# Kernel tuning notes

Measured on AMD Instinct MI355X. Metric: run time of the kernel, lower is better.

## Reference

```python
import jax, jax.numpy as jnp
import numpy as np

PAD_MAG = 1e12
EPS = 1e-7  # matches prev_step.add_(1e-07) in the torch code


def setup_inputs() -> dict:
    key = jax.random.key(0)
    k1, k2, k3, k4 = jax.random.split(key, 4)
    B, txt_T, mel_T, n_mel = 16, 320, 2000, 80
    mu_logvar = jax.random.normal(k1, (B, txt_T, 2 * n_mel), dtype=jnp.float32)
    melspec = jax.random.normal(k2, (B, n_mel, mel_T), dtype=jnp.float32)
    text_lengths = jax.random.randint(k3, (B,), txt_T // 2, txt_T + 1).astype(jnp.int32)
    mel_lengths = jax.random.randint(k4, (B,), mel_T // 2, mel_T + 1).astype(jnp.int32)
    return {"mu_logvar": mu_logvar, "melspec": melspec,
            "text_lengths": text_lengths, "mel_lengths": mel_lengths}


def _log_prob_matrix(mu_logvar, melspec):
    # exponential[b,j,t] = -0.5 * mean_c( (x[b,t,c]-mu[b,j,c])^2 / exp(logvar) + logvar )
    # avoiding the [B,txt_T,mel_T,n_mel] broadcast the torch code materializes.
    n_mel = melspec.shape[1]
    mu = mu_logvar[:, :, :n_mel]          # [B, txt_T, n_mel]
    logvar = mu_logvar[:, :, n_mel:]      # [B, txt_T, n_mel]
    x = jnp.swapaxes(melspec, 1, 2)       # [B, mel_T, n_mel]
    inv_var = jnp.exp(-logvar)
    xx = jnp.einsum('btc,bjc->bjt', x * x, inv_var)
    xm = jnp.einsum('btc,bjc->bjt', x, mu * inv_var)
    mm = jnp.sum(mu * mu * inv_var + logvar, axis=2)  # [B, txt_T]
    return (-0.5 / n_mel) * (xx - 2.0 * xm + mm[:, :, None])  # [B, txt_T, mel_T]


def _forward_dp(log_prob, text_lengths, mel_lengths):
    # monotonic alignment forward algorithm (logsumexp DP over mel frames)
    B, txt_T, mel_T = log_prob.shape
    # carry = log_alpha column of size txt_T+1 (row 0 is the -inf pad row)
    init = jnp.full((B, txt_T + 1), -PAD_MAG, log_prob.dtype)
    init = init.at[:, 1].set(log_prob[:, 0, 0])

    def step(a, lp):  # a: [B, txt_T+1], lp: [B, txt_T]
        prev = jnp.stack([a[:, 1:], a[:, :-1]], axis=-1) + EPS
        tail = jax.nn.logsumexp(prev, axis=-1) + lp      # [B, txt_T]
        a_new = jnp.concatenate(
            [jnp.full((B, 1), -PAD_MAG, a.dtype), tail], axis=1)
        return a_new, tail

    lps = jnp.moveaxis(log_prob[:, :, 1:], 2, 0)         # [mel_T-1, B, txt_T]
    _, tails = jax.lax.scan(step, init, lps)             # [mel_T-1, B, txt_T]
    log_alpha = jnp.concatenate([init[None, :, 1:], tails], axis=0)  # [mel_T, B, txt_T]
    log_alpha = jnp.moveaxis(log_alpha, 0, 2)            # [B, txt_T, mel_T]

    bidx = jnp.arange(B)
    alpha_last = log_alpha[bidx, text_lengths - 1, mel_lengths - 1]
    alpha_last = alpha_last / mel_lengths.astype(log_alpha.dtype)
    return -jnp.mean(alpha_last)


def reference(mu_logvar, melspec, text_lengths, mel_lengths):
    log_prob = _log_prob_matrix(mu_logvar, melspec)
    mdn_loss = _forward_dp(log_prob, text_lengths, mel_lengths)
    return (mdn_loss, log_prob)
```

## Files before the change

### kernel.cpp

```cpp
#include <hip/hip_runtime.h>

#define BATCH 16
#define TXT   320
#define NMELC 80
#define MELT  2000
#define PADM  1.0e12f
#define EPSC  1e-7f
#define L2E   1.4426950408889634f
#define LN2   0.6931471805599453f
#define EPSL2 1.4426950e-7f

__global__ __launch_bounds__(256) void lp_kernel(
    const float* __restrict__ mlv,
    const float* __restrict__ ms,
    float* __restrict__ out_lp)
{
    __shared__ float Gt[16][64];
    __shared__ float Ft[16][256];
    __shared__ float bias_s[64];
    __shared__ float bias_p[256];

    const int b   = blockIdx.z;
    const int j0  = blockIdx.y * 64;
    const int t0  = blockIdx.x * 256;
    const int tid = threadIdx.x;
    const float s = -0.00625f;

    const float* mlv_b = mlv + (size_t)b * TXT * 160;
    const float* ms_b  = ms  + (size_t)b * NMELC * MELT;

    {
        const int jj = tid >> 2;
        const int q  = tid & 3;
        const float* p = mlv_b + (size_t)(j0 + jj) * 160 + q * 20;
        float part = 0.f;
        #pragma unroll
        for (int c = 0; c < 20; ++c) {
            float mu = p[c];
            float lv = p[c + 80];
            float iv = __expf(-lv);
            part += mu * mu * iv + lv;
        }
        bias_p[tid] = part;
    }
    __syncthreads();
    if (tid < 64) {
        float v = bias_p[tid * 4] + bias_p[tid * 4 + 1] +
                  bias_p[tid * 4 + 2] + bias_p[tid * 4 + 3];
        bias_s[tid] = s * v;
    }

    float acc[8][8];
    #pragma unroll
    for (int i = 0; i < 8; ++i)
        #pragma unroll
        for (int k = 0; k < 8; ++k) acc[i][k] = 0.f;

    const int jg = tid >> 5;
    const int tg = tid & 31;

    for (int kc = 0; kc < 10; ++kc) {
        const int c0 = kc * 8;
        __syncthreads();
        #pragma unroll
        for (int i = 0; i < 2; ++i) {
            int f   = tid + i * 256;
            int cr  = f >> 6;
            int col = f & 63;
            float mu = mlv_b[(size_t)(j0 + col) * 160 + (c0 + cr)];
            float lv = mlv_b[(size_t)(j0 + col) * 160 + (80 + c0 + cr)];
            float iv = __expf(-lv);
            Gt[cr][col]     = s * iv;
            Gt[cr + 8][col] = -2.f * s * mu * iv;
        }
        #pragma unroll
        for (int i = 0; i < 2; ++i) {
            int f   = tid + i * 256;
            int row = f >> 6;
            int c4  = f & 63;
            int t   = t0 + c4 * 4;
            float4 v = (t + 3 < MELT)
                ? *(const float4*)&ms_b[(size_t)(c0 + row) * MELT + t]
                : make_float4(0.f, 0.f, 0.f, 0.f);
            *(float4*)&Ft[row][c4 * 4] =
                make_float4(v.x * v.x, v.y * v.y, v.z * v.z, v.w * v.w);
            *(float4*)&Ft[row + 8][c4 * 4] = v;
        }
        __syncthreads();
        #pragma unroll
        for (int k = 0; k < 16; ++k) {
            float4 g0 = *(const float4*)&Gt[k][jg * 8];
            float4 g1 = *(const float4*)&Gt[k][jg * 8 + 4];
            float4 f0 = *(const float4*)&Ft[k][tg * 8];
            float4 f1 = *(const float4*)&Ft[k][tg * 8 + 4];
            float ga[8] = {g0.x, g0.y, g0.z, g0.w, g1.x, g1.y, g1.z, g1.w};
            float fa[8] = {f0.x, f0.y, f0.z, f0.w, f1.x, f1.y, f1.z, f1.w};
            #pragma unroll
            for (int ji = 0; ji < 8; ++ji)
                #pragma unroll
                for (int ti = 0; ti < 8; ++ti)
                    acc[ji][ti] = fmaf(ga[ji], fa[ti], acc[ji][ti]);
        }
    }

    #pragma unroll
    for (int ji = 0; ji < 8; ++ji) {
        int j = j0 + jg * 8 + ji;
        float bs = bias_s[jg * 8 + ji];
        float* orow = out_lp + (size_t)(b * TXT + j) * MELT;
        #pragma unroll
        for (int ti = 0; ti < 8; ++ti) {
            int t = t0 + tg * 8 + ti;
            if (t < MELT) orow[t] = acc[ji][ti] + bs;
        }
    }
}

__device__ __forceinline__ float dpp_shr1(float x) {
    return __int_as_float(__builtin_amdgcn_update_dpp(
        0, __float_as_int(x), 0x138 , 0xF, 0xF, false));
}

__global__ __launch_bounds__(192, 1) void dp_kernel(
    const float* __restrict__ lp,
    const int* __restrict__ tlen,
    const int* __restrict__ mlen,
    float* __restrict__ res,
    float* __restrict__ out0)
{
    __shared__ float bnd[2][2056];
    __shared__ int   prog[2];

    const int b    = blockIdx.x;
    const int tid  = threadIdx.x;
    const int w    = tid >> 6;
    const int l    = tid & 63;
    const int tend = mlen[b] - 1;
    const int tl   = tlen[b];

    if (tid < 2) prog[tid] = 0;

    int j0c = 2 * tid; if (j0c > 318) j0c = 318;
    const float* r0 = lp + (size_t)(b * TXT + j0c) * MELT;
    const float* r1 = r0 + MELT;

    float A1 = (tid == 0) ? lp[(size_t)b * TXT * MELT] * L2E : -PADM;
    float A2 = -PADM;
    float A1F = A1, A2F = A2;

    if (l == 63 && w < 2) bnd[w][0] = -PADM;
    __syncthreads();

    if (w == 2 && tl < 257) return;

    float ptA2 = -PADM, ptB2 = -PADM;
    const bool is0     = (l == 0);
    const bool isPub   = (l == 63) && (w < 2);
    const bool hasRing = (w > 0);
    int seen = 0;

    const int imax = tend + 63;

    float PA[16], PB[16], PC[16];
    #pragma unroll
    for (int q = 0; q < 8; ++q) { PA[2*q] = r0[1 + q - l]; PA[2*q+1] = r1[1 + q - l]; }
    #pragma unroll
    for (int q = 0; q < 8; ++q) { PB[2*q] = r0[9 + q - l]; PB[2*q+1] = r1[9 + q - l]; }
    #pragma unroll
    for (int q = 0; q < 16; ++q) PA[q] = fmaf(PA[q], L2E, EPSL2);

    const float* p0 = r0 + 17 - l;
    const float* p1 = r1 + 17 - l;

#define RING_RD(BQ_, T0_)                                                    \
    {                                                                        \
        float4 r0_ = *(const float4*)&bnd[w - 1][T0_];                       \
        float4 r1_ = *(const float4*)&bnd[w - 1][(T0_) + 4];                 \
        BQ_[0]=r0_.x; BQ_[1]=r0_.y; BQ_[2]=r0_.z; BQ_[3]=r0_.w;              \
        BQ_[4]=r1_.x; BQ_[5]=r1_.y; BQ_[6]=r1_.z; BQ_[7]=r1_.w;              \
    }
#define RING_POLL(NEED_)                                                     \
    if (seen < (NEED_)) {                                                    \
        int tgt_ = (NEED_) + 32;                                             \
        if (tgt_ > tend - 1) tgt_ = tend - 1;                                \
        if (tgt_ < (NEED_)) tgt_ = (NEED_);                                  \
        volatile int* pv_ = &prog[w - 1];                                    \
        int v_ = *pv_;                                                       \
        while (v_ < tgt_) { __builtin_amdgcn_s_sleep(1); v_ = *pv_; }        \
        seen = v_;                                                           \
        __asm__ volatile("" ::: "memory");                                   \
    }

    float bqC[8];
    if (hasRing) {
        RING_POLL(7)
        RING_RD(bqC, 0)
    } else {
        #pragma unroll
        for (int q = 0; q < 8; ++q) bqC[q] = -PADM;
    }

#define STEP2(Pc_, q_, AQ_)                                                  \
    {                                                                        \
        float pt_ = is0 ? bqC[q_] : ptA2;                                    \
        float m1_ = fmaxf(A1, pt_);                                          \
        float d1_ = A1 - pt_;                                                \
        float e1_ = __builtin_amdgcn_exp2f(-fabsf(d1_));                     \
        float g1_ = __builtin_amdgcn_logf(1.0f + e1_);                       \
        float n1_ = m1_ + g1_ + Pc_[2 * q_];                                 \
        float m2_ = fmaxf(A2, A1);                                           \
        float d2_ = A2 - A1;                                                 \
        float e2_ = __builtin_amdgcn_exp2f(-fabsf(d2_));                     \
        float g2_ = __builtin_amdgcn_logf(1.0f + e2_);                       \
        float n2_ = m2_ + g2_ + Pc_[2 * q_ + 1];                             \
        float ns_ = dpp_shr1(n2_);                                           \
        ptA2 = ptB2; ptB2 = ns_;                                             \
        A1 = n1_; A2 = n2_; AQ_ = n2_;                                       \
    }

#define GROUP2_S(Pc_, Pm_, Pl_, I0_)                                         \
{                                                                            \
    float bqN[8];                                                            \
    if (hasRing) {                                                           \
        const int nt0_ = (I0_) + 7;                                          \
        RING_POLL(nt0_ + 7)                                                  \
        RING_RD(bqN, nt0_)                                                   \
    } else {                                                                 \
        _Pragma("unroll") for (int q_=0;q_<8;++q_) bqN[q_] = -PADM;          \
    }                                                                        \
    _Pragma("unroll") for (int q_=0;q_<8;++q_) {                             \
        Pl_[2*q_] = p0[q_]; Pl_[2*q_+1] = p1[q_];                            \
    }                                                                        \
    float aq2[8];                                                            \
    _Pragma("unroll")                                                        \
    for (int q_=0;q_<8;++q_) STEP2(Pc_, q_, aq2[q_])                         \
    if (isPub) {                                                             \
        const int t63_ = (I0_) - 63;                                         \
        if (t63_ >= 1) {                                                     \
            _Pragma("unroll") for (int q_=0;q_<8;++q_)                       \
                bnd[w][t63_ + q_] = aq2[q_];                                 \
        } else {                                                             \
            _Pragma("unroll") for (int q_=0;q_<8;++q_)                       \
                if (t63_ + q_ >= 1) bnd[w][t63_ + q_] = aq2[q_];             \
        }                                                                    \
        __asm__ volatile("" ::: "memory");          \
        int pgv_ = t63_ + 7;                                                 \
        if (pgv_ >= 1) prog[w] = pgv_;                                       \
    }                                                                        \
    p0 += 8; p1 += 8;                                                        \
    _Pragma("unroll") for (int q_=0;q_<16;++q_)                              \
        Pm_[q_] = fmaf(Pm_[q_], L2E, EPSL2);                                 \
    _Pragma("unroll") for (int q_=0;q_<8;++q_) bqC[q_] = bqN[q_];            \
}

#define GROUP2_T(Pc_, Pm_, Pl_, I0_)                                         \
{                                                                            \
    float bqN[8];                                                            \
    if (hasRing) {                                                           \
        const int nt0_ = (I0_) + 7;                                          \
        int need_ = nt0_ + 7; if (need_ > tend - 1) need_ = tend - 1;        \
        RING_POLL(need_)                                                     \
        const int rb_ = nt0_ > 2048 ? 2048 : nt0_;                           \
        RING_RD(bqN, rb_)                                                    \
    } else {                                                                 \
        _Pragma("unroll") for (int q_=0;q_<8;++q_) bqN[q_] = -PADM;          \
    }                                                                        \
    _Pragma("unroll") for (int q_=0;q_<8;++q_) {                             \
        int t_ = (I0_) + 16 + q_ - l;                                        \
        t_ = t_ < 0 ? 0 : (t_ > tend ? tend : t_);                           \
        Pl_[2*q_] = r0[t_]; Pl_[2*q_+1] = r1[t_];                            \
    }                                                                        \
    float aq2[8];                                                            \
    const int vt_ = (I0_) - l;                                               \
    _Pragma("unroll")                                                        \
    for (int q_=0;q_<8;++q_) {                                               \
        STEP2(Pc_, q_, aq2[q_])                                              \
        bool c_ = (vt_ + q_ == tend);                                        \
        A1F = c_ ? A1 : A1F;                                                 \
        A2F = c_ ? A2 : A2F;                                                 \
    }                                                                        \
    if (isPub) {                                                             \
        const int t63_ = (I0_) - 63;                                         \
        _Pragma("unroll") for (int q_=0;q_<8;++q_) {                         \
            int tq_ = t63_ + q_;                                             \
            if (tq_ >= 1 && tq_ <= tend) bnd[w][tq_] = aq2[q_];              \
        }                                                                    \
        __asm__ volatile("" ::: "memory");                                   \
        int pgv_ = t63_ + 7; if (pgv_ > tend) pgv_ = tend;                   \
        if (pgv_ >= 1) prog[w] = pgv_;                                       \
    }                                                                        \
    _Pragma("unroll") for (int q_=0;q_<16;++q_)                              \
        Pm_[q_] = fmaf(Pm_[q_], L2E, EPSL2);                                 \
    _Pragma("unroll") for (int q_=0;q_<8;++q_) bqC[q_] = bqN[q_];            \
}

    int i0 = 1;
    const int sEnd = tend - 23;
    int ph = 0;
    while (i0 <= sEnd) {
        GROUP2_S(PA, PB, PC, i0); i0 += 8;
        if (i0 > sEnd) { ph = 1; break; }
        GROUP2_S(PB, PC, PA, i0); i0 += 8;
        if (i0 > sEnd) { ph = 2; break; }
        GROUP2_S(PC, PA, PB, i0); i0 += 8;
    }
    if (ph == 1) {
        #pragma unroll
        for (int q = 0; q < 16; ++q) {
            float tmp = PA[q]; PA[q] = PB[q]; PB[q] = PC[q]; PC[q] = tmp;
        }
    } else if (ph == 2) {
        #pragma unroll
        for (int q = 0; q < 16; ++q) {
            float tmp = PA[q]; PA[q] = PC[q]; PC[q] = PB[q]; PB[q] = tmp;
        }
    }
    while (i0 <= imax) {
        GROUP2_T(PA, PB, PC, i0); i0 += 8;
        if (i0 > imax) break;
        GROUP2_T(PB, PC, PA, i0); i0 += 8;
        if (i0 > imax) break;
        GROUP2_T(PC, PA, PB, i0); i0 += 8;
    }

#undef GROUP2_S
#undef GROUP2_T
#undef STEP2
#undef RING_RD
#undef RING_POLL

    if (tid == ((tl - 1) >> 1)) {
        float Af = ((tl - 1) & 1) ? A2F : A1F;
        float v = Af * LN2 / (float)(tend + 1);
        if (res) res[b] = v;
        else     atomicAdd(out0, -v / (float)BATCH);
    }
}

__global__ void zero1_kernel(float* out0) { out0[0] = 0.f; }

__global__ void fin_kernel(const float* __restrict__ res, float* __restrict__ out0)
{
    int l = threadIdx.x;
    float v = (l < BATCH) ? res[l] : 0.f;
    #pragma unroll
    for (int off = 32; off; off >>= 1) v += __shfl_down(v, off);
    if (l == 0) out0[0] = -(v / (float)BATCH);
}

extern "C" void kernel_launch(void* const* d_in, const int* in_sizes, int n_in,
                              void* d_out, int out_size, void* d_ws, size_t ws_size,
                              hipStream_t stream)
{
    const float* mlv = (const float*)d_in[0];
    const float* ms  = (const float*)d_in[1];
    const int*   tl  = (const int*)d_in[2];
    const int*   ml  = (const int*)d_in[3];
    float* out    = (float*)d_out;
    float* out_lp = out + 1;

    bool res_ok = ws_size >= 64;
    float* res = res_ok ? (float*)d_ws : nullptr;

    dim3 gA(8, 5, 16);
    lp_kernel<<<gA, 256, 0, stream>>>(mlv, ms, out_lp);

    if (!res_ok) zero1_kernel<<<1, 1, 0, stream>>>(out);
    dp_kernel<<<BATCH, 192, 0, stream>>>(out_lp, tl, ml, res, out);
    if (res_ok) fin_kernel<<<1, 64, 0, stream>>>(res, out);
}
```

Measured before the change: 244.7 us.

## Split DP into forward and backward half passes meeting in the middle

Replaces the single sequential forward DP per batch with two concurrent passes: a forward pass over the first half of mel frames and a backward pass from the end over the second half. A small kernel then combines the two half-results with a logsumexp over text positions. This roughly halves the serial chain length of the latency-bound DP and doubles the blocks from 16 to 32. The cost is extra workspace, two extra small kernels, and added numerical/indexing risk in the reverse-pass initialization and the boundary subtraction.

```diff
diff --git a/kernel.cpp b/kernel.cpp
--- a/kernel.cpp
+++ b/kernel.cpp
@@ -5,7 +5,6 @@
 #define NMELC 80
 #define MELT  2000
 #define PADM  1.0e12f
-#define EPSC  1e-7f
 #define L2E   1.4426950408889634f
 #define LN2   0.6931471805599453f
 #define EPSL2 1.4426950e-7f
@@ -121,68 +120,81 @@
         0, __float_as_int(x), 0x138 , 0xF, 0xF, false));
 }
 
-__global__ __launch_bounds__(192, 1) void dp_kernel(
-    const float* __restrict__ lp,
-    const int* __restrict__ tlen,
-    const int* __restrict__ mlen,
-    float* __restrict__ res,
-    float* __restrict__ out0)
-{
-    __shared__ float bnd[2][2056];
+__device__ __forceinline__ void dp_pass(
+    const float* __restrict__ lp, int b, int dir, int tend, int tl,
+    float* __restrict__ Fout, float* __restrict__ out0)
+{
+    __shared__ float bnd[2][2080];
     __shared__ int   prog[2];
 
-    const int b    = blockIdx.x;
-    const int tid  = threadIdx.x;
-    const int w    = tid >> 6;
-    const int l    = tid & 63;
-    const int tend = mlen[b] - 1;
-    const int tl   = tlen[b];
+    const int tid = threadIdx.x;
+    const int w   = tid >> 6;
+    const int l   = tid & 63;
+    const int tm    = tend >> 1;
+    const int steps = Fout ? (dir ? (tend - tm) : tm) : tend;
+    const int t0c   = dir ? tend : 0;
+    const int dsgn  = dir ? -1 : 1;
 
     if (tid < 2) prog[tid] = 0;
 
-    int j0c = 2 * tid; if (j0c > 318) j0c = 318;
-    const float* r0 = lp + (size_t)(b * TXT + j0c) * MELT;
-    const float* r1 = r0 + MELT;
-
-    float A1 = (tid == 0) ? lp[(size_t)b * TXT * MELT] * L2E : -PADM;
-    float A2 = -PADM;
+    const int tc = tid < 160 ? tid : 159;
+    const int R0 = dir ? (319 - 2 * tc) : (2 * tc);
+    const int R1 = dir ? (318 - 2 * tc) : (2 * tc + 1);
+    const float* r0 = lp + ((size_t)b * TXT + R0) * MELT;
+    const float* r1 = lp + ((size_t)b * TXT + R1) * MELT;
+
+    float A1 = -PADM, A2 = -PADM;
+    if (!dir) {
+        if (tid == 0) A1 = lp[(size_t)b * TXT * MELT] * L2E;
+    } else {
+        const int jin = 320 - tl;
+        const float vin =
+            fmaf(lp[((size_t)b * TXT + (tl - 1)) * MELT + tend], L2E, EPSL2);
+        if (tid == (jin >> 1)) { if (jin & 1) A2 = vin; else A1 = vin; }
+    }
     float A1F = A1, A2F = A2;
 
-    if (l == 63 && w < 2) bnd[w][0] = -PADM;
+    if (l == 63 && w < 2) bnd[w][0] = A2;
     __syncthreads();
-
-    if (w == 2 && tl < 257) return;
-
-    float ptA2 = -PADM, ptB2 = -PADM;
+    if (tid >= 192) return;
+
+    float ptA2 = -PADM;
+    float ptB2 = dpp_shr1(A2);
     const bool is0     = (l == 0);
     const bool isPub   = (l == 63) && (w < 2);
     const bool hasRing = (w > 0);
     int seen = 0;
-
-    const int imax = tend + 63;
+    const int imax = steps + 63;
 
     float PA[16], PB[16], PC[16];
     #pragma unroll
-    for (int q = 0; q < 8; ++q) { PA[2*q] = r0[1 + q - l]; PA[2*q+1] = r1[1 + q - l]; }
-    #pragma unroll
-    for (int q = 0; q < 8; ++q) { PB[2*q] = r0[9 + q - l]; PB[2*q+1] = r1[9 + q - l]; }
+    for (int q = 0; q < 8; ++q) {
+        int s_ = 1 + q - l;
+        int c_ = t0c + dsgn * s_;
+        c_ = c_ < 0 ? 0 : (c_ > MELT - 1 ? MELT - 1 : c_);
+        PA[2 * q] = r0[c_]; PA[2 * q + 1] = r1[c_];
+    }
+    #pragma unroll
+    for (int q = 0; q < 8; ++q) {
+        int s_ = 9 + q - l;
+        int c_ = t0c + dsgn * s_;
+        c_ = c_ < 0 ? 0 : (c_ > MELT - 1 ? MELT - 1 : c_);
+        PB[2 * q] = r0[c_]; PB[2 * q + 1] = r1[c_];
+    }
     #pragma unroll
     for (int q = 0; q < 16; ++q) PA[q] = fmaf(PA[q], L2E, EPSL2);
-
-    const float* p0 = r0 + 17 - l;
-    const float* p1 = r1 + 17 - l;
 
 #define RING_RD(BQ_, T0_)                                                    \
     {                                                                        \
-        float4 r0_ = *(const float4*)&bnd[w - 1][T0_];                       \
-        float4 r1_ = *(const float4*)&bnd[w - 1][(T0_) + 4];                 \
-        BQ_[0]=r0_.x; BQ_[1]=r0_.y; BQ_[2]=r0_.z; BQ_[3]=r0_.w;              \
-        BQ_[4]=r1_.x; BQ_[5]=r1_.y; BQ_[6]=r1_.z; BQ_[7]=r1_.w;              \
+        float4 q0_ = *(const float4*)&bnd[w - 1][T0_];                       \
+        float4 q1_ = *(const float4*)&bnd[w - 1][(T0_) + 4];                 \
+        BQ_[0]=q0_.x; BQ_[1]=q0_.y; BQ_[2]=q0_.z; BQ_[3]=q0_.w;              \
+        BQ_[4]=q1_.x; BQ_[5]=q1_.y; BQ_[6]=q1_.z; BQ_[7]=q1_.w;              \
     }
 #define RING_POLL(NEED_)                                                     \
     if (seen < (NEED_)) {                                                    \
         int tgt_ = (NEED_) + 32;                                             \
-        if (tgt_ > tend - 1) tgt_ = tend - 1;                                \
+        if (tgt_ > steps - 1) tgt_ = steps - 1;                              \
         if (tgt_ < (NEED_)) tgt_ = (NEED_);                                  \
         volatile int* pv_ = &prog[w - 1];                                    \
         int v_ = *pv_;                                                       \
@@ -193,100 +205,65 @@
 
     float bqC[8];
     if (hasRing) {
-        RING_POLL(7)
+        int need0 = 7; if (need0 > steps - 1) need0 = steps - 1;
+        RING_POLL(need0)
         RING_RD(bqC, 0)
     } else {
         #pragma unroll
         for (int q = 0; q < 8; ++q) bqC[q] = -PADM;
     }
 
-#define STEP2(Pc_, q_, AQ_)                                                  \
-    {                                                                        \
+#define GROUPX(Pc_, Pm_, Pl_, I0_)                                           \
+{                                                                            \
+    float bqN[8];                                                            \
+    if (hasRing) {                                                           \
+        int need_ = (I0_) + 14;                                              \
+        if (need_ > steps - 1) need_ = steps - 1;                            \
+        RING_POLL(need_)                                                     \
+        int rb_ = (I0_) + 7; if (rb_ > 2048) rb_ = 2048;                     \
+        RING_RD(bqN, rb_)                                                    \
+    } else {                                                                 \
+        _Pragma("unroll") for (int q_=0;q_<8;++q_) bqN[q_] = -PADM;          \
+    }                                                                        \
+    _Pragma("unroll") for (int q_=0;q_<8;++q_) {                             \
+        int s_ = (I0_) + 16 + q_ - l;                                        \
+        int c_ = t0c + dsgn * s_;                                            \
+        c_ = c_ < 0 ? 0 : (c_ > MELT - 1 ? MELT - 1 : c_);                   \
+        Pl_[2*q_] = r0[c_]; Pl_[2*q_+1] = r1[c_];                            \
+    }                                                                        \
+    float aq2[8];                                                            \
+    const int vt_ = (I0_) - l;                                               \
+    _Pragma("unroll") for (int q_=0;q_<8;++q_) {                             \
         float pt_ = is0 ? bqC[q_] : ptA2;                                    \
         float m1_ = fmaxf(A1, pt_);                                          \
         float d1_ = A1 - pt_;                                                \
         float e1_ = __builtin_amdgcn_exp2f(-fabsf(d1_));                     \
         float g1_ = __builtin_amdgcn_logf(1.0f + e1_);                       \
-        float n1_ = m1_ + g1_ + Pc_[2 * q_];                                 \
+        float n1_ = m1_ + g1_ + Pc_[2*q_];                                   \
         float m2_ = fmaxf(A2, A1);                                           \
         float d2_ = A2 - A1;                                                 \
         float e2_ = __builtin_amdgcn_exp2f(-fabsf(d2_));                     \
         float g2_ = __builtin_amdgcn_logf(1.0f + e2_);                       \
-        float n2_ = m2_ + g2_ + Pc_[2 * q_ + 1];                             \
-        float ns_ = dpp_shr1(n2_);                                           \
+        float n2_ = m2_ + g2_ + Pc_[2*q_+1];                                 \
+        bool go_ = (vt_ + q_ >= 1);                                          \
+        A1 = go_ ? n1_ : A1;                                                 \
+        A2 = go_ ? n2_ : A2;                                                 \
+        float ns_ = dpp_shr1(A2);                                            \
         ptA2 = ptB2; ptB2 = ns_;                                             \
-        A1 = n1_; A2 = n2_; AQ_ = n2_;                                       \
-    }
-
-#define GROUP2_S(Pc_, Pm_, Pl_, I0_)                                         \
-{                                                                            \
-    float bqN[8];                                                            \
-    if (hasRing) {                                                           \
-        const int nt0_ = (I0_) + 7;                                          \
-        RING_POLL(nt0_ + 7)                                                  \
-        RING_RD(bqN, nt0_)                                                   \
-    } else {                                                                 \
-        _Pragma("unroll") for (int q_=0;q_<8;++q_) bqN[q_] = -PADM;          \
-    }                                                                        \
-    _Pragma("unroll") for (int q_=0;q_<8;++q_) {                             \
-        Pl_[2*q_] = p0[q_]; Pl_[2*q_+1] = p1[q_];                            \
-    }                                                                        \
-    float aq2[8];                                                            \
-    _Pragma("unroll")                                                        \
-    for (int q_=0;q_<8;++q_) STEP2(Pc_, q_, aq2[q_])                         \
-    if (isPub) {                                                             \
-        const int t63_ = (I0_) - 63;                                         \
-        if (t63_ >= 1) {                                                     \
-            _Pragma("unroll") for (int q_=0;q_<8;++q_)                       \
-                bnd[w][t63_ + q_] = aq2[q_];                                 \
-        } else {                                                             \
-            _Pragma("unroll") for (int q_=0;q_<8;++q_)                       \
-                if (t63_ + q_ >= 1) bnd[w][t63_ + q_] = aq2[q_];             \
-        }                                                                    \
-        __asm__ volatile("" ::: "memory");          \
-        int pgv_ = t63_ + 7;                                                 \
-        if (pgv_ >= 1) prog[w] = pgv_;                                       \
-    }                                                                        \
-    p0 += 8; p1 += 8;                                                        \
-    _Pragma("unroll") for (int q_=0;q_<16;++q_)                              \
-        Pm_[q_] = fmaf(Pm_[q_], L2E, EPSL2);                                 \
-    _Pragma("unroll") for (int q_=0;q_<8;++q_) bqC[q_] = bqN[q_];            \
-}
-
-#define GROUP2_T(Pc_, Pm_, Pl_, I0_)                                         \
-{                                                                            \
-    float bqN[8];                                                            \
-    if (hasRing) {                                                           \
-        const int nt0_ = (I0_) + 7;                                          \
-        int need_ = nt0_ + 7; if (need_ > tend - 1) need_ = tend - 1;        \
-        RING_POLL(need_)                                                     \
-        const int rb_ = nt0_ > 2048 ? 2048 : nt0_;                           \
-        RING_RD(bqN, rb_)                                                    \
-    } else {                                                                 \
-        _Pragma("unroll") for (int q_=0;q_<8;++q_) bqN[q_] = -PADM;          \
-    }                                                                        \
-    _Pragma("unroll") for (int q_=0;q_<8;++q_) {                             \
-        int t_ = (I0_) + 16 + q_ - l;                                        \
-        t_ = t_ < 0 ? 0 : (t_ > tend ? tend : t_);                           \
-        Pl_[2*q_] = r0[t_]; Pl_[2*q_+1] = r1[t_];                            \
-    }                                                                        \
-    float aq2[8];                                                            \
-    const int vt_ = (I0_) - l;                                               \
-    _Pragma("unroll")                                                        \
-    for (int q_=0;q_<8;++q_) {                                               \
-        STEP2(Pc_, q_, aq2[q_])                                              \
-        bool c_ = (vt_ + q_ == tend);                                        \
-        A1F = c_ ? A1 : A1F;                                                 \
-        A2F = c_ ? A2 : A2F;                                                 \
+        aq2[q_] = A2;                                                        \
+        bool cF_ = (vt_ + q_ == steps);                                      \
+        A1F = cF_ ? A1 : A1F;                                                \
+        A2F = cF_ ? A2 : A2F;                                                \
     }                                                                        \
     if (isPub) {                                                             \
         const int t63_ = (I0_) - 63;                                         \
         _Pragma("unroll") for (int q_=0;q_<8;++q_) {                         \
             int tq_ = t63_ + q_;                                             \
-            if (tq_ >= 1 && tq_ <= tend) bnd[w][tq_] = aq2[q_];              \
+            if (tq_ >= 1 && tq_ <= 2056) bnd[w][tq_] = aq2[q_];              \
         }                                                                    \
         __asm__ volatile("" ::: "memory");                                   \
-        int pgv_ = t63_ + 7; if (pgv_ > tend) pgv_ = tend;                   \
+        int pgv_ = t63_ + 7;                                                 \
+        if (pgv_ > steps - 1) pgv_ = steps - 1;                              \
         if (pgv_ >= 1) prog[w] = pgv_;                                       \
     }                                                                        \
     _Pragma("unroll") for (int q_=0;q_<16;++q_)                              \
@@ -295,51 +272,86 @@
 }
 
     int i0 = 1;
-    const int sEnd = tend - 23;
-    int ph = 0;
-    while (i0 <= sEnd) {
-        GROUP2_S(PA, PB, PC, i0); i0 += 8;
-        if (i0 > sEnd) { ph = 1; break; }
-        GROUP2_S(PB, PC, PA, i0); i0 += 8;
-        if (i0 > sEnd) { ph = 2; break; }
-        GROUP2_S(PC, PA, PB, i0); i0 += 8;
-    }
-    if (ph == 1) {
-        #pragma unroll
-        for (int q = 0; q < 16; ++q) {
-            float tmp = PA[q]; PA[q] = PB[q]; PB[q] = PC[q]; PC[q] = tmp;
-        }
-    } else if (ph == 2) {
-        #pragma unroll
-        for (int q = 0; q < 16; ++q) {
-            float tmp = PA[q]; PA[q] = PC[q]; PC[q] = PB[q]; PB[q] = tmp;
-        }
-    }
     while (i0 <= imax) {
-        GROUP2_T(PA, PB, PC, i0); i0 += 8;
-        if (i0 > imax) break;
-        GROUP2_T(PB, PC, PA, i0); i0 += 8;
-        if (i0 > imax) break;
-        GROUP2_T(PC, PA, PB, i0); i0 += 8;
-    }
-
-#undef GROUP2_S
-#undef GROUP2_T
-#undef STEP2
+        GROUPX(PA, PB, PC, i0); i0 += 8; if (i0 > imax) break;
+        GROUPX(PB, PC, PA, i0); i0 += 8; if (i0 > imax) break;
+        GROUPX(PC, PA, PB, i0); i0 += 8;
+    }
+
+#undef GROUPX
 #undef RING_RD
 #undef RING_POLL
 
-    if (tid == ((tl - 1) >> 1)) {
-        float Af = ((tl - 1) & 1) ? A2F : A1F;
-        float v = Af * LN2 / (float)(tend + 1);
-        if (res) res[b] = v;
-        else     atomicAdd(out0, -v / (float)BATCH);
-    }
-}
-
-__global__ void zero1_kernel(float* out0) { out0[0] = 0.f; }
-
-__global__ void fin_kernel(const float* __restrict__ res, float* __restrict__ out0)
+    if (!Fout) {
+        if (tid == ((tl - 1) >> 1)) {
+            float Af = ((tl - 1) & 1) ? A2F : A1F;
+            atomicAdd(out0, -(Af * LN2 / (float)(tend + 1)) / (float)BATCH);
+        }
+        return;
+    }
+    if (tid < 160) {
+        if (!dir) {
+            *(float2*)&Fout[(size_t)b * TXT + 2 * tid] =
+                make_float2(A1F, A2F);
+        } else {
+            float q0 = fmaf(r0[tm], L2E, EPSL2);
+            float q1 = fmaf(r1[tm], L2E, EPSL2);
+            *(float2*)&Fout[(size_t)b * TXT + (318 - 2 * tid)] =
+                make_float2(A2F - q1, A1F - q0);
+        }
+    }
+}
+
+__global__ __launch_bounds__(256, 1) void dp2_kernel(
+    const float* __restrict__ lp, const int* __restrict__ tlen,
+    const int* __restrict__ mlen, float* __restrict__ F,
+    float* __restrict__ G)
+{
+    const int blk = blockIdx.x;
+    const int b   = blk & 15;
+    const int dir = blk >> 4;
+    dp_pass(lp, b, dir, mlen[b] - 1, tlen[b], dir ? G : F, nullptr);
+}
+
+__global__ __launch_bounds__(256, 1) void dp_fb_kernel(
+    const float* __restrict__ lp, const int* __restrict__ tlen,
+    const int* __restrict__ mlen, float* __restrict__ out0)
+{
+    const int b = blockIdx.x;
+    dp_pass(lp, b, 0, mlen[b] - 1, tlen[b], nullptr, out0);
+}
+
+__global__ void fin1_kernel(const float* __restrict__ F,
+                            const float* __restrict__ G,
+                            const int* __restrict__ mlen,
+                            float* __restrict__ res)
+{
+    const int b = blockIdx.x;
+    const int l = threadIdx.x;
+    float v[5];
+    float m = -3.0e38f;
+    #pragma unroll
+    for (int k = 0; k < 5; ++k) {
+        int j = 5 * l + k;
+        v[k] = F[(size_t)b * TXT + j] + G[(size_t)b * TXT + j];
+        m = fmaxf(m, v[k]);
+    }
+    #pragma unroll
+    for (int o = 32; o; o >>= 1) m = fmaxf(m, __shfl_xor(m, o));
+    float s = 0.f;
+    #pragma unroll
+    for (int k = 0; k < 5; ++k) {
+        float d = v[k] - m;
+        d = d < -120.f ? -120.f : d;
+        s += __builtin_amdgcn_exp2f(d);
+    }
+    #pragma unroll
+    for (int o = 32; o; o >>= 1) s += __shfl_xor(s, o);
+    if (l == 0)
+        res[b] = (m + __builtin_amdgcn_logf(s)) * LN2 / (float)mlen[b];
+}
+
+__global__ void fin2_kernel(const float* __restrict__ res, float* __restrict__ out0)
 {
     int l = threadIdx.x;
     float v = (l < BATCH) ? res[l] : 0.f;
@@ -347,6 +359,8 @@
     for (int off = 32; off; off >>= 1) v += __shfl_down(v, off);
     if (l == 0) out0[0] = -(v / (float)BATCH);
 }
+
+__global__ void zero1_kernel(float* out0) { out0[0] = 0.f; }
 
 extern "C" void kernel_launch(void* const* d_in, const int* in_sizes, int n_in,
                               void* d_out, int out_size, void* d_ws, size_t ws_size,
@@ -359,13 +373,21 @@
     float* out    = (float*)d_out;
     float* out_lp = out + 1;
 
-    bool res_ok = ws_size >= 64;
-    float* res = res_ok ? (float*)d_ws : nullptr;
+    const size_t need = 256 + (size_t)2 * BATCH * TXT * sizeof(float);
+    bool ok = ws_size >= need;
+    float* res = (float*)d_ws;
+    float* F   = (float*)((char*)d_ws + 256);
+    float* G   = F + (size_t)BATCH * TXT;
 
     dim3 gA(8, 5, 16);
     lp_kernel<<<gA, 256, 0, stream>>>(mlv, ms, out_lp);
 
-    if (!res_ok) zero1_kernel<<<1, 1, 0, stream>>>(out);
-    dp_kernel<<<BATCH, 192, 0, stream>>>(out_lp, tl, ml, res, out);
-    if (res_ok) fin_kernel<<<1, 64, 0, stream>>>(res, out);
-}
+    if (ok) {
+        dp2_kernel<<<32, 256, 0, stream>>>(out_lp, tl, ml, F, G);
+        fin1_kernel<<<BATCH, 64, 0, stream>>>(F, G, ml, res);
+        fin2_kernel<<<1, 64, 0, stream>>>(res, out);
+    } else {
+        zero1_kernel<<<1, 1, 0, stream>>>(out);
+        dp_fb_kernel<<<BATCH, 256, 0, stream>>>(out_lp, tl, ml, out);
+    }
+}
```

New measurement: 258.0 us. +5.4%, slower.

## Compute log-prob GEMM with bf16 MFMA instead of fp32 FMA

Applied to the files above, without the earlier changes.

Replaces the scalar fp32 outer-product GEMM in lp_kernel with bf16 MFMA 16x16x32 instructions. Operands are converted to bf16 and staged in shared memory in a k-packed layout, and the t tile is halved so the grid doubles. This cuts ALU time for the log-prob matrix. The cost is bf16 rounding of x^2, x and the inverse-variance terms in the expanded form, and the xx - 2xm cancellation may lose enough accuracy to break tolerance. The DP kernel, which probably dominates total time, is unchanged.

```diff
diff --git a/kernel.cpp b/kernel.cpp
--- a/kernel.cpp
+++ b/kernel.cpp
@@ -5,24 +5,32 @@
 #define NMELC 80
 #define MELT  2000
 #define PADM  1.0e12f
-#define EPSC  1e-7f
 #define L2E   1.4426950408889634f
 #define LN2   0.6931471805599453f
 #define EPSL2 1.4426950e-7f
+
+typedef __attribute__((ext_vector_type(8))) short bf16x8;
+typedef __attribute__((ext_vector_type(4))) float f32x4;
+
+__device__ __forceinline__ short f2bf(float x) {
+    unsigned u = __float_as_uint(x);
+    unsigned r = (u + 0x7FFFu + ((u >> 16) & 1u)) >> 16;
+    return (short)r;
+}
 
 __global__ __launch_bounds__(256) void lp_kernel(
     const float* __restrict__ mlv,
     const float* __restrict__ ms,
     float* __restrict__ out_lp)
 {
-    __shared__ float Gt[16][64];
-    __shared__ float Ft[16][256];
+    __shared__ short Ash[20][64][8];
+    __shared__ short Bsh[20][128][8];
+    __shared__ float bias_p[256];
     __shared__ float bias_s[64];
-    __shared__ float bias_p[256];
 
     const int b   = blockIdx.z;
     const int j0  = blockIdx.y * 64;
-    const int t0  = blockIdx.x * 256;
+    const int t0  = blockIdx.x * 128;
     const int tid = threadIdx.x;
     const float s = -0.00625f;
 
@@ -50,68 +58,72 @@
         bias_s[tid] = s * v;
     }
 
-    float acc[8][8];
-    #pragma unroll
-    for (int i = 0; i < 8; ++i)
-        #pragma unroll
-        for (int k = 0; k < 8; ++k) acc[i][k] = 0.f;
-
-    const int jg = tid >> 5;
-    const int tg = tid & 31;
-
-    for (int kc = 0; kc < 10; ++kc) {
-        const int c0 = kc * 8;
-        __syncthreads();
-        #pragma unroll
-        for (int i = 0; i < 2; ++i) {
-            int f   = tid + i * 256;
-            int cr  = f >> 6;
-            int col = f & 63;
-            float mu = mlv_b[(size_t)(j0 + col) * 160 + (c0 + cr)];
-            float lv = mlv_b[(size_t)(j0 + col) * 160 + (80 + c0 + cr)];
-            float iv = __expf(-lv);
-            Gt[cr][col]     = s * iv;
-            Gt[cr + 8][col] = -2.f * s * mu * iv;
-        }
-        #pragma unroll
-        for (int i = 0; i < 2; ++i) {
-            int f   = tid + i * 256;
-            int row = f >> 6;
-            int c4  = f & 63;
-            int t   = t0 + c4 * 4;
-            float4 v = (t + 3 < MELT)
-                ? *(const float4*)&ms_b[(size_t)(c0 + row) * MELT + t]
-                : make_float4(0.f, 0.f, 0.f, 0.f);
-            *(float4*)&Ft[row][c4 * 4] =
-                make_float4(v.x * v.x, v.y * v.y, v.z * v.z, v.w * v.w);
-            *(float4*)&Ft[row + 8][c4 * 4] = v;
-        }
-        __syncthreads();
-        #pragma unroll
-        for (int k = 0; k < 16; ++k) {
-            float4 g0 = *(const float4*)&Gt[k][jg * 8];
-            float4 g1 = *(const float4*)&Gt[k][jg * 8 + 4];
-            float4 f0 = *(const float4*)&Ft[k][tg * 8];
-            float4 f1 = *(const float4*)&Ft[k][tg * 8 + 4];
-            float ga[8] = {g0.x, g0.y, g0.z, g0.w, g1.x, g1.y, g1.z, g1.w};
-            float fa[8] = {f0.x, f0.y, f0.z, f0.w, f1.x, f1.y, f1.z, f1.w};
+    #pragma unroll
+    for (int pass = 0; pass < 20; ++pass) {
+        int idx = pass * 256 + tid;
+        int j = idx / 80;
+        int c = idx - j * 80;
+        float mu = mlv_b[(size_t)(j0 + j) * 160 + c];
+        float lv = mlv_b[(size_t)(j0 + j) * 160 + 80 + c];
+        float iv = __expf(-lv);
+        Ash[c >> 3][j][c & 7]        = f2bf(s * iv);
+        Ash[10 + (c >> 3)][j][c & 7] = f2bf(-2.f * s * mu * iv);
+    }
+    #pragma unroll
+    for (int pass = 0; pass < 10; ++pass) {
+        int c   = pass * 8 + (tid >> 5);
+        int t4i = tid & 31;
+        int t   = t0 + t4i * 4;
+        float xv[4];
+        if (t + 3 < MELT) {
+            float4 v = *(const float4*)&ms_b[(size_t)c * MELT + t];
+            xv[0] = v.x; xv[1] = v.y; xv[2] = v.z; xv[3] = v.w;
+        } else {
             #pragma unroll
-            for (int ji = 0; ji < 8; ++ji)
-                #pragma unroll
-                for (int ti = 0; ti < 8; ++ti)
-                    acc[ji][ti] = fmaf(ga[ji], fa[ti], acc[ji][ti]);
-        }
-    }
-
-    #pragma unroll
-    for (int ji = 0; ji < 8; ++ji) {
-        int j = j0 + jg * 8 + ji;
-        float bs = bias_s[jg * 8 + ji];
-        float* orow = out_lp + (size_t)(b * TXT + j) * MELT;
-        #pragma unroll
-        for (int ti = 0; ti < 8; ++ti) {
-            int t = t0 + tg * 8 + ti;
-            if (t < MELT) orow[t] = acc[ji][ti] + bs;
+            for (int i = 0; i < 4; ++i)
+                xv[i] = (t + i < MELT) ? ms_b[(size_t)c * MELT + t + i] : 0.f;
+        }
+        #pragma unroll
+        for (int i = 0; i < 4; ++i) {
+            Bsh[c >> 3][t4i * 4 + i][c & 7]        = f2bf(xv[i] * xv[i]);
+            Bsh[10 + (c >> 3)][t4i * 4 + i][c & 7] = f2bf(xv[i]);
+        }
+    }
+    __syncthreads();
+
+    const int wv = tid >> 6;
+    const int l  = tid & 63;
+    const int lr = l & 15;
+    const int lg = l >> 4;
+
+    f32x4 acc[8];
+    #pragma unroll
+    for (int f = 0; f < 8; ++f) acc[f] = (f32x4){0.f, 0.f, 0.f, 0.f};
+
+    #pragma unroll
+    for (int ks = 0; ks < 5; ++ks) {
+        const int kb = ks * 4 + lg;
+        bf16x8 a = *(const bf16x8*)&Ash[kb][wv * 16 + lr][0];
+        #pragma unroll
+        for (int f = 0; f < 8; ++f) {
+            bf16x8 bb = *(const bf16x8*)&Bsh[kb][f * 16 + lr][0];
+            acc[f] = __builtin_amdgcn_mfma_f32_16x16x32_bf16(a, bb, acc[f],
+                                                             0, 0, 0);
+        }
+    }
+
+    float bs[4];
+    #pragma unroll
+    for (int r = 0; r < 4; ++r) bs[r] = bias_s[wv * 16 + lg * 4 + r];
+    #pragma unroll
+    for (int f = 0; f < 8; ++f) {
+        int t = t0 + f * 16 + lr;
+        if (t < MELT) {
+            #pragma unroll
+            for (int r = 0; r < 4; ++r) {
+                int j = j0 + wv * 16 + lg * 4 + r;
+                out_lp[((size_t)b * TXT + j) * MELT + t] = acc[f][r] + bs[r];
+            }
         }
     }
 }
@@ -174,10 +186,10 @@
 
 #define RING_RD(BQ_, T0_)                                                    \
     {                                                                        \
-        float4 r0_ = *(const float4*)&bnd[w - 1][T0_];                       \
-        float4 r1_ = *(const float4*)&bnd[w - 1][(T0_) + 4];                 \
-        BQ_[0]=r0_.x; BQ_[1]=r0_.y; BQ_[2]=r0_.z; BQ_[3]=r0_.w;              \
-        BQ_[4]=r1_.x; BQ_[5]=r1_.y; BQ_[6]=r1_.z; BQ_[7]=r1_.w;              \
+        float4 q0_ = *(const float4*)&bnd[w - 1][T0_];                       \
+        float4 q1_ = *(const float4*)&bnd[w - 1][(T0_) + 4];                 \
+        BQ_[0]=q0_.x; BQ_[1]=q0_.y; BQ_[2]=q0_.z; BQ_[3]=q0_.w;              \
+        BQ_[4]=q1_.x; BQ_[5]=q1_.y; BQ_[6]=q1_.z; BQ_[7]=q1_.w;              \
     }
 #define RING_POLL(NEED_)                                                     \
     if (seen < (NEED_)) {                                                    \
@@ -362,7 +374,7 @@
     bool res_ok = ws_size >= 64;
     float* res = res_ok ? (float*)d_ws : nullptr;
 
-    dim3 gA(8, 5, 16);
+    dim3 gA(16, 5, 16);
     lp_kernel<<<gA, 256, 0, stream>>>(mlv, ms, out_lp);
 
     if (!res_ok) zero1_kernel<<<1, 1, 0, stream>>>(out);
```

After: 208.5 us. 1.17x faster.
